# Kernel optimization log

Measured on AMD Instinct MI355X. Metric: run time of the kernel, lower is better.

## Reference

```python
import jax, jax.numpy as jnp
import numpy as np

N_QUBITS = 8
DEPTH = 2
N_STATES = 1 << N_QUBITS  # 256
BATCH = (2, 32768)


def _cz_phase(n_qubits: int) -> np.ndarray:
    """Diagonal phase of nearest-neighbor CZ gates over all basis states."""
    basis = np.arange(1 << n_qubits)
    phase = np.ones(1 << n_qubits, dtype=np.float32)
    for left in range(n_qubits - 1):
        both_one = ((basis >> left) & 1 == 1) & ((basis >> (left + 1)) & 1 == 1)
        phase = np.where(both_one, -phase, phase)
    return phase


def setup_inputs() -> dict:
    key = jax.random.key(0)
    k1, k2 = jax.random.split(key)
    projected_features = jax.random.normal(k1, BATCH + (N_QUBITS,), dtype=jnp.float32)
    theta = 0.05 * jax.random.normal(k2, (DEPTH, N_QUBITS), dtype=jnp.float32)
    input_scale = jnp.ones((N_QUBITS,), dtype=jnp.float32)
    return {"projected_features": projected_features, "theta": theta, "input_scale": input_scale}


def reference(projected_features, theta, input_scale):
    n_qubits = projected_features.shape[-1]
    depth = theta.shape[0]
    n_states = 1 << n_qubits
    batch_shape = projected_features.shape[:-1]
    dtype = projected_features.dtype

    cz_phase = jnp.asarray(_cz_phase(n_qubits), dtype=dtype)

    # |0...0> initial state
    state = jnp.zeros(batch_shape + (n_states,), dtype=dtype).at[..., 0].set(1.0)
    bounded = jnp.tanh(projected_features) * np.pi  # [..., n_qubits]

    for layer in range(depth):
        for q in range(n_qubits):
            angle = bounded[..., q] * input_scale[q] + theta[layer, q]  # [...]
            c = jnp.cos(angle * 0.5)[..., None, None]
            s = jnp.sin(angle * 0.5)[..., None, None]
            # basis index = high * 2^(q+1) + bit_q * 2^q + low; split out bit_q
            r = state.reshape(batch_shape + (n_states >> (q + 1), 2, 1 << q))
            s0 = r[..., 0, :]
            s1 = r[..., 1, :]
            new = jnp.stack([c * s0 - s * s1, s * s0 + c * s1], axis=-2)
            state = new.reshape(batch_shape + (n_states,))
        state = state * cz_phase

    norm = jnp.linalg.norm(state, axis=-1, keepdims=True)
    return state / jnp.maximum(norm, 1e-12)
```

## Files before the change

kernel.cpp:

```cpp
#include <hip/hip_runtime.h>
#include <math.h>

#define PI_F 3.14159265358979323846f

typedef float    f32x4 __attribute__((ext_vector_type(4)));
typedef _Float16 h2    __attribute__((ext_vector_type(2)));

#if __has_builtin(__builtin_elementwise_fma)
#define FMA2(a, b, c) __builtin_elementwise_fma((a), (b), (c))
#else
#define FMA2(a, b, c) ((a) * (b) + (c))
#endif

__device__ __forceinline__ h2 pkrtz(float a, float b) {
    return __builtin_bit_cast(h2, __builtin_amdgcn_cvt_pkrtz(a, b));
}

template <int PAT>
__device__ __forceinline__ h2 swzh(h2 x) {
    return __builtin_bit_cast(h2, __builtin_amdgcn_ds_swizzle(__builtin_bit_cast(int, x), PAT));
}
#define BCAST_PAT(q) (((((q) & 3) | (((q) & 4) << 1)) << 5) | 0x14)

template <int CTRL>
__device__ __forceinline__ h2 dpph(h2 x) {
    int i = __builtin_bit_cast(int, x);
    return __builtin_bit_cast(h2, __builtin_amdgcn_update_dpp(i, i, CTRL, 0xF, 0xF, false));
}
#define DPP_XOR1 0xB1
#define DPP_XOR2 0x4E
#define DPP_XOR8 0x128

__device__ __forceinline__ h2 hswap(h2 a) {
    return __builtin_shufflevector(a, a, 1, 0);
}
__device__ __forceinline__ h2 splat_lo(h2 a) { h2 r = { a[0], a[0] }; return r; }
__device__ __forceinline__ h2 splat_hi(h2 a) { h2 r = { a[1], a[1] }; return r; }

#define SLO_MASK 0x4748B848u

__global__ __launch_bounds__(256) void qenc_kernel(
    const float* __restrict__ pf,
    const float* __restrict__ theta,
    const float* __restrict__ scale,
    float* __restrict__ out,
    int B)
{
    const int lane = threadIdx.x & 63;
    const int wid  = threadIdx.x >> 6;
    const int sub  = (lane & 3) | ((lane >> 1) & 4);
    const int g    = ((lane >> 2) & 1) | ((lane >> 3) & 6);

    __shared__ __align__(16) float lds[4 * 2048];
    float* base = lds + wid * 2048;

    const int grp   = blockIdx.x * 4 + wid;
    const int bwave = grp * 8;
    const int b     = bwave + g;
    if (b >= B) return;

    float x  = pf[(size_t)b * 8 + sub];
    float e  = __expf(2.f * x);
    float th = 1.f - 2.f / (e + 1.f);
    float b2 = th * (0.5f * PI_F) * scale[sub];
    float h0a = b2 + 0.5f * theta[sub];
    float h1a = b2 + 0.5f * theta[8 + sub];
    float c0 = __cosf(h0a), s0 = __sinf(h0a);
    float cL = __cosf(h1a), sL = __sinf(h1a);
    h2 cs0 = pkrtz(c0, s0);
    h2 csl = pkrtz(cL, sL);

    h2 k0 = swzh<BCAST_PAT(0)>(cs0), k1 = swzh<BCAST_PAT(1)>(cs0);
    h2 k2 = swzh<BCAST_PAT(2)>(cs0), k3 = swzh<BCAST_PAT(3)>(cs0);
    h2 k4 = swzh<BCAST_PAT(4)>(cs0), k5 = swzh<BCAST_PAT(5)>(cs0);
    h2 k6 = swzh<BCAST_PAT(6)>(cs0), k7 = swzh<BCAST_PAT(7)>(cs0);
    float KC0 = (float)k0[0], KS0 = (float)k0[1];
    float KC1 = (float)k1[0], KS1 = (float)k1[1];
    float KC2 = (float)k2[0], KS2 = (float)k2[1];
    float KC3 = (float)k3[0], KS3 = (float)k3[1];
    float KC4 = (float)k4[0], KS4 = (float)k4[1];
    float KC5 = (float)k5[0], KS5 = (float)k5[1];
    float KC6 = (float)k6[0], KS6 = (float)k6[1];
    float KC7 = (float)k7[0], KS7 = (float)k7[1];

    const float A  = (__popc(sub & (sub >> 1) & 3) & 1) ? -1.f : 1.f;
    const float A4 = (sub & 1) ? -A : A;

    float f5 = (sub & 1) ? KS5 : KC5;
    float f6 = (sub & 2) ? KS6 : KC6;
    float f7 = (sub & 4) ? KS7 : KC7;
    float Phi  = f5 * f6 * f7 * A;
    float KS4L = (sub & 1) ? -KS4 : KS4;

    float a00 = KC0 * KC1, a10 = KS0 * KC1, a01 = KC0 * KS1, a11 = KS0 * KS1;
    const float uu[4] = { Phi * a00, Phi * a10, Phi * a01, Phi * a11 };
    float t23_0 = KC2 * KC3, t23_1 = KS2 * KC3, t23_2 = KC2 * KS3, t23_3 = KS2 * KS3;
    const float wwl[8] = { t23_0 * KC4,  t23_1 * KC4,  t23_2 * KC4,  t23_3 * KC4,
                           t23_0 * KS4L, t23_1 * KS4L, t23_2 * KS4L, t23_3 * KS4L };

    h2 P[16];
#pragma unroll
    for (int j = 0; j < 16; ++j) {
        float lo = uu[2 * (j & 1)]     * wwl[j >> 1];
        float hi = uu[2 * (j & 1) + 1] * wwl[j >> 1];
        if ((SLO_MASK >> (2 * j)) & 1)     lo = -lo;
        if ((SLO_MASK >> (2 * j + 1)) & 1) hi = -hi;
        P[j] = pkrtz(lo, hi);
    }

    h2 q0 = swzh<BCAST_PAT(0)>(csl), q1 = swzh<BCAST_PAT(1)>(csl);
    h2 q2 = swzh<BCAST_PAT(2)>(csl), q3 = swzh<BCAST_PAT(3)>(csl);
    h2 q4 = swzh<BCAST_PAT(4)>(csl), q5 = swzh<BCAST_PAT(5)>(csl);
    h2 q6 = swzh<BCAST_PAT(6)>(csl), q7 = swzh<BCAST_PAT(7)>(csl);

#define PK_INTRA(SBJ, cs)                                             \
    do {                                                              \
        h2 c2 = splat_lo(cs), s2 = splat_hi(cs);                      \
        _Pragma("unroll")                                             \
        for (int bse = 0; bse < 16; bse += 2 * (SBJ)) {               \
            _Pragma("unroll")                                         \
            for (int off = 0; off < (SBJ); ++off) {                   \
                int j0 = bse + off, j1 = j0 + (SBJ);                  \
                h2 a = P[j0], bb = P[j1];                             \
                P[j0] = FMA2(c2, a, -(s2 * bb));                      \
                P[j1] = FMA2(c2, bb, s2 * a);                         \
            }                                                         \
        }                                                             \
    } while (0)

#define PK_CROSS(CTRL, BIT, cs)                                       \
    do {                                                              \
        h2 c2 = splat_lo(cs), s2 = splat_hi(cs);                      \
        h2 se = (sub & (BIT)) ? s2 : -s2;                             \
        _Pragma("unroll")                                             \
        for (int j = 0; j < 16; ++j) {                                \
            h2 t = dpph<CTRL>(P[j]);                                  \
            P[j] = FMA2(c2, P[j], se * t);                            \
        }                                                             \
    } while (0)

    PK_INTRA(1, q1);
    PK_INTRA(2, q2);
    PK_INTRA(4, q3);
    PK_INTRA(8, q4);
    PK_CROSS(DPP_XOR1, 1, q5);
    PK_CROSS(DPP_XOR2, 2, q6);
    PK_CROSS(DPP_XOR8, 4, q7);
    {
        h2 c2 = splat_lo(q0);
        _Float16 sh = q0[1];
        h2 sm = { (_Float16)(-sh), sh };
#pragma unroll
        for (int j = 0; j < 16; ++j)
            P[j] = FMA2(c2, P[j], sm * hswap(P[j]));
    }

#pragma unroll
    for (int j = 0; j < 16; ++j) {
        float bA = (j < 8) ? A : A4;
        h2 sv = { (_Float16)(((SLO_MASK >> (2 * j)) & 1) ? -bA : bA),
                  (_Float16)(((SLO_MASK >> (2 * j + 1)) & 1) ? -bA : bA) };
        P[j] = P[j] * sv;
    }

#pragma unroll
    for (int k = 0; k < 8; ++k) {
        int c  = sub * 8 + k;
        int cp = c ^ sub;
        f32x4 w = { (float)P[2 * k][0], (float)P[2 * k][1],
                    (float)P[2 * k + 1][0], (float)P[2 * k + 1][1] };
        *reinterpret_cast<f32x4*>(base + g * 256 + cp * 4) = w;
    }
    const int cr = lane ^ (lane >> 3);
#pragma unroll
    for (int j = 0; j < 8; ++j) {
        f32x4 t = *reinterpret_cast<const f32x4*>(base + j * 256 + cr * 4);
        __builtin_nontemporal_store(t,
            reinterpret_cast<f32x4*>(out + (size_t)(bwave + j) * 256 + lane * 4));
    }
}

extern "C" void kernel_launch(void* const* d_in, const int* in_sizes, int n_in,
                              void* d_out, int out_size, void* d_ws, size_t ws_size,
                              hipStream_t stream) {
    const float* pf    = (const float*)d_in[0];
    const float* theta = (const float*)d_in[1];
    const float* scale = (const float*)d_in[2];
    float* out = (float*)d_out;

    int B = in_sizes[0] / 8;
    int grid = (B / 8 + 3) / 4;
    qenc_kernel<<<grid, 256, 0, stream>>>(pf, theta, scale, out, B);
}
```

Baseline: 18.15 us.

## Map one batch element per wave with four amplitudes per lane

Reorganizes the work so each wave handles a single batch element, with every lane holding four amplitudes, instead of eight elements per wave at sixteen amplitudes per lane. Gates on higher qubits become cross-lane exchanges (DPP, ds_swizzle, shfl_xor) rather than in-register butterflies. This removes the LDS transpose staging and cuts register pressure, so writes go straight to global memory as coalesced 16-byte nontemporal stores. In exchange it launches eight times as many waves, adds more cross-lane operations per element, and drops the bounds check on the batch size.

```diff
diff --git a/kernel.cpp b/kernel.cpp
--- a/kernel.cpp
+++ b/kernel.cpp
@@ -20,7 +20,9 @@
 __device__ __forceinline__ h2 swzh(h2 x) {
     return __builtin_bit_cast(h2, __builtin_amdgcn_ds_swizzle(__builtin_bit_cast(int, x), PAT));
 }
-#define BCAST_PAT(q) (((((q) & 3) | (((q) & 4) << 1)) << 5) | 0x14)
+#define BCASTALL_PAT(q) ((q) << 5)
+#define SWZ_XOR4  0x101F
+#define SWZ_XOR16 0x401F
 
 template <int CTRL>
 __device__ __forceinline__ h2 dpph(h2 x) {
@@ -31,13 +33,15 @@
 #define DPP_XOR2 0x4E
 #define DPP_XOR8 0x128
 
+__device__ __forceinline__ h2 xor32h(h2 x) {
+    return __builtin_bit_cast(h2, __shfl_xor(__builtin_bit_cast(int, x), 32, 64));
+}
+
 __device__ __forceinline__ h2 hswap(h2 a) {
     return __builtin_shufflevector(a, a, 1, 0);
 }
 __device__ __forceinline__ h2 splat_lo(h2 a) { h2 r = { a[0], a[0] }; return r; }
 __device__ __forceinline__ h2 splat_hi(h2 a) { h2 r = { a[1], a[1] }; return r; }
-
-#define SLO_MASK 0x4748B848u
 
 __global__ __launch_bounds__(256) void qenc_kernel(
     const float* __restrict__ pf,
@@ -48,16 +52,8 @@
 {
     const int lane = threadIdx.x & 63;
     const int wid  = threadIdx.x >> 6;
-    const int sub  = (lane & 3) | ((lane >> 1) & 4);
-    const int g    = ((lane >> 2) & 1) | ((lane >> 3) & 6);
-
-    __shared__ __align__(16) float lds[4 * 2048];
-    float* base = lds + wid * 2048;
-
-    const int grp   = blockIdx.x * 4 + wid;
-    const int bwave = grp * 8;
-    const int b     = bwave + g;
-    if (b >= B) return;
+    const int b    = blockIdx.x * 4 + wid;
+    const int sub  = lane & 7;
 
     float x  = pf[(size_t)b * 8 + sub];
     float e  = __expf(2.f * x);
@@ -65,119 +61,74 @@
     float b2 = th * (0.5f * PI_F) * scale[sub];
     float h0a = b2 + 0.5f * theta[sub];
     float h1a = b2 + 0.5f * theta[8 + sub];
-    float c0 = __cosf(h0a), s0 = __sinf(h0a);
-    float cL = __cosf(h1a), sL = __sinf(h1a);
-    h2 cs0 = pkrtz(c0, s0);
-    h2 csl = pkrtz(cL, sL);
+    h2 cs0 = pkrtz(__cosf(h0a), __sinf(h0a));
+    h2 csl = pkrtz(__cosf(h1a), __sinf(h1a));
 
-    h2 k0 = swzh<BCAST_PAT(0)>(cs0), k1 = swzh<BCAST_PAT(1)>(cs0);
-    h2 k2 = swzh<BCAST_PAT(2)>(cs0), k3 = swzh<BCAST_PAT(3)>(cs0);
-    h2 k4 = swzh<BCAST_PAT(4)>(cs0), k5 = swzh<BCAST_PAT(5)>(cs0);
-    h2 k6 = swzh<BCAST_PAT(6)>(cs0), k7 = swzh<BCAST_PAT(7)>(cs0);
-    float KC0 = (float)k0[0], KS0 = (float)k0[1];
-    float KC1 = (float)k1[0], KS1 = (float)k1[1];
-    float KC2 = (float)k2[0], KS2 = (float)k2[1];
-    float KC3 = (float)k3[0], KS3 = (float)k3[1];
-    float KC4 = (float)k4[0], KS4 = (float)k4[1];
-    float KC5 = (float)k5[0], KS5 = (float)k5[1];
-    float KC6 = (float)k6[0], KS6 = (float)k6[1];
-    float KC7 = (float)k7[0], KS7 = (float)k7[1];
+    h2 k0 = swzh<BCASTALL_PAT(0)>(cs0), k1 = swzh<BCASTALL_PAT(1)>(cs0);
+    h2 k2 = swzh<BCASTALL_PAT(2)>(cs0), k3 = swzh<BCASTALL_PAT(3)>(cs0);
+    h2 k4 = swzh<BCASTALL_PAT(4)>(cs0), k5 = swzh<BCASTALL_PAT(5)>(cs0);
+    h2 k6 = swzh<BCASTALL_PAT(6)>(cs0), k7 = swzh<BCASTALL_PAT(7)>(cs0);
+    h2 q0 = swzh<BCASTALL_PAT(0)>(csl), q1 = swzh<BCASTALL_PAT(1)>(csl);
+    h2 q2 = swzh<BCASTALL_PAT(2)>(csl), q3 = swzh<BCASTALL_PAT(3)>(csl);
+    h2 q4 = swzh<BCASTALL_PAT(4)>(csl), q5 = swzh<BCASTALL_PAT(5)>(csl);
+    h2 q6 = swzh<BCASTALL_PAT(6)>(csl), q7 = swzh<BCASTALL_PAT(7)>(csl);
 
-    const float A  = (__popc(sub & (sub >> 1) & 3) & 1) ? -1.f : 1.f;
-    const float A4 = (sub & 1) ? -A : A;
+    float G;
+    G  = (lane & 1)  ? (float)k2[1] : (float)k2[0];
+    G *= (lane & 2)  ? (float)k3[1] : (float)k3[0];
+    G *= (lane & 4)  ? (float)k4[1] : (float)k4[0];
+    G *= (lane & 8)  ? (float)k5[1] : (float)k5[0];
+    G *= (lane & 16) ? (float)k6[1] : (float)k6[0];
+    G *= (lane & 32) ? (float)k7[1] : (float)k7[0];
 
-    float f5 = (sub & 1) ? KS5 : KC5;
-    float f6 = (sub & 2) ? KS6 : KC6;
-    float f7 = (sub & 4) ? KS7 : KC7;
-    float Phi  = f5 * f6 * f7 * A;
-    float KS4L = (sub & 1) ? -KS4 : KS4;
+    float SL  = (__popc(lane & (lane >> 1) & 0x1F) & 1) ? -1.f : 1.f;
+    float lam = (lane & 1) ? -1.f : 1.f;
 
-    float a00 = KC0 * KC1, a10 = KS0 * KC1, a01 = KC0 * KS1, a11 = KS0 * KS1;
-    const float uu[4] = { Phi * a00, Phi * a10, Phi * a01, Phi * a11 };
-    float t23_0 = KC2 * KC3, t23_1 = KS2 * KC3, t23_2 = KC2 * KS3, t23_3 = KS2 * KS3;
-    const float wwl[8] = { t23_0 * KC4,  t23_1 * KC4,  t23_2 * KC4,  t23_3 * KC4,
-                           t23_0 * KS4L, t23_1 * KS4L, t23_2 * KS4L, t23_3 * KS4L };
+    float Gs = G * SL;
+    float gc = Gs * (float)k1[0];
+    float gs = Gs * (float)k1[1] * lam;
+    h2 P0 = pkrtz(gc * (float)k0[0],  gc * (float)k0[1]);
+    h2 P1 = pkrtz(gs * (float)k0[0], -gs * (float)k0[1]);
 
-    h2 P[16];
-#pragma unroll
-    for (int j = 0; j < 16; ++j) {
-        float lo = uu[2 * (j & 1)]     * wwl[j >> 1];
-        float hi = uu[2 * (j & 1) + 1] * wwl[j >> 1];
-        if ((SLO_MASK >> (2 * j)) & 1)     lo = -lo;
-        if ((SLO_MASK >> (2 * j + 1)) & 1) hi = -hi;
-        P[j] = pkrtz(lo, hi);
-    }
-
-    h2 q0 = swzh<BCAST_PAT(0)>(csl), q1 = swzh<BCAST_PAT(1)>(csl);
-    h2 q2 = swzh<BCAST_PAT(2)>(csl), q3 = swzh<BCAST_PAT(3)>(csl);
-    h2 q4 = swzh<BCAST_PAT(4)>(csl), q5 = swzh<BCAST_PAT(5)>(csl);
-    h2 q6 = swzh<BCAST_PAT(6)>(csl), q7 = swzh<BCAST_PAT(7)>(csl);
-
-#define PK_INTRA(SBJ, cs)                                             \
+#define XGATE(EXCH, BIT, cs)                                          \
     do {                                                              \
         h2 c2 = splat_lo(cs), s2 = splat_hi(cs);                      \
-        _Pragma("unroll")                                             \
-        for (int bse = 0; bse < 16; bse += 2 * (SBJ)) {               \
-            _Pragma("unroll")                                         \
-            for (int off = 0; off < (SBJ); ++off) {                   \
-                int j0 = bse + off, j1 = j0 + (SBJ);                  \
-                h2 a = P[j0], bb = P[j1];                             \
-                P[j0] = FMA2(c2, a, -(s2 * bb));                      \
-                P[j1] = FMA2(c2, bb, s2 * a);                         \
-            }                                                         \
-        }                                                             \
+        h2 se = (lane & (BIT)) ? s2 : -s2;                            \
+        h2 t0 = EXCH(P0), t1 = EXCH(P1);                              \
+        P0 = FMA2(c2, P0, se * t0);                                   \
+        P1 = FMA2(c2, P1, se * t1);                                   \
     } while (0)
 
-#define PK_CROSS(CTRL, BIT, cs)                                       \
-    do {                                                              \
-        h2 c2 = splat_lo(cs), s2 = splat_hi(cs);                      \
-        h2 se = (sub & (BIT)) ? s2 : -s2;                             \
-        _Pragma("unroll")                                             \
-        for (int j = 0; j < 16; ++j) {                                \
-            h2 t = dpph<CTRL>(P[j]);                                  \
-            P[j] = FMA2(c2, P[j], se * t);                            \
-        }                                                             \
-    } while (0)
+    XGATE(dpph<DPP_XOR1>,  1,  q2);
+    XGATE(dpph<DPP_XOR2>,  2,  q3);
+    XGATE(swzh<SWZ_XOR4>,  4,  q4);
+    XGATE(dpph<DPP_XOR8>,  8,  q5);
+    XGATE(swzh<SWZ_XOR16>, 16, q6);
+    XGATE(xor32h,          32, q7);
 
-    PK_INTRA(1, q1);
-    PK_INTRA(2, q2);
-    PK_INTRA(4, q3);
-    PK_INTRA(8, q4);
-    PK_CROSS(DPP_XOR1, 1, q5);
-    PK_CROSS(DPP_XOR2, 2, q6);
-    PK_CROSS(DPP_XOR8, 4, q7);
+    {
+        h2 c2 = splat_lo(q1), s2 = splat_hi(q1);
+        h2 a = P0, bb = P1;
+        P0 = FMA2(c2, a, -(s2 * bb));
+        P1 = FMA2(c2, bb, s2 * a);
+    }
     {
         h2 c2 = splat_lo(q0);
         _Float16 sh = q0[1];
         h2 sm = { (_Float16)(-sh), sh };
-#pragma unroll
-        for (int j = 0; j < 16; ++j)
-            P[j] = FMA2(c2, P[j], sm * hswap(P[j]));
+        P0 = FMA2(c2, P0, sm * hswap(P0));
+        P1 = FMA2(c2, P1, sm * hswap(P1));
     }
 
-#pragma unroll
-    for (int j = 0; j < 16; ++j) {
-        float bA = (j < 8) ? A : A4;
-        h2 sv = { (_Float16)(((SLO_MASK >> (2 * j)) & 1) ? -bA : bA),
-                  (_Float16)(((SLO_MASK >> (2 * j + 1)) & 1) ? -bA : bA) };
-        P[j] = P[j] * sv;
-    }
+    float SLl = SL * lam;
+    h2 z0 = { (_Float16)SL,  (_Float16)SL };
+    h2 z1 = { (_Float16)SLl, (_Float16)(-SLl) };
+    P0 = P0 * z0;
+    P1 = P1 * z1;
 
-#pragma unroll
-    for (int k = 0; k < 8; ++k) {
-        int c  = sub * 8 + k;
-        int cp = c ^ sub;
-        f32x4 w = { (float)P[2 * k][0], (float)P[2 * k][1],
-                    (float)P[2 * k + 1][0], (float)P[2 * k + 1][1] };
-        *reinterpret_cast<f32x4*>(base + g * 256 + cp * 4) = w;
-    }
-    const int cr = lane ^ (lane >> 3);
-#pragma unroll
-    for (int j = 0; j < 8; ++j) {
-        f32x4 t = *reinterpret_cast<const f32x4*>(base + j * 256 + cr * 4);
-        __builtin_nontemporal_store(t,
-            reinterpret_cast<f32x4*>(out + (size_t)(bwave + j) * 256 + lane * 4));
-    }
+    f32x4 o = { (float)P0[0], (float)P0[1], (float)P1[0], (float)P1[1] };
+    __builtin_nontemporal_store(o,
+        reinterpret_cast<f32x4*>(out + (size_t)b * 256 + lane * 4));
 }
 
 extern "C" void kernel_launch(void* const* d_in, const int* in_sizes, int n_in,
@@ -189,6 +140,6 @@
     float* out = (float*)d_out;
 
     int B = in_sizes[0] / 8;
-    int grid = (B / 8 + 3) / 4;
+    int grid = B / 4;
     qenc_kernel<<<grid, 256, 0, stream>>>(pf, theta, scale, out, B);
 }
```

Measured after the change: 23.57 us. 29.8% more time.
